# Optimization experiments

Hardware: AMD Instinct MI355X
Metric: run time of the kernel (lower is better)

The kernel has to match this reference:

```python
import jax, jax.numpy as jnp
import numpy as np

NODES, NFEAT = 128, 256


def setup_inputs() -> dict:
    key = jax.random.key(0)
    k1, k2, k3, k4, k5, k6 = jax.random.split(key, 6)
    B = 512
    x = jax.random.normal(k1, (B, NODES, NFEAT), dtype=jnp.float32)
    adj = jax.random.uniform(k2, (B, NODES, NODES), dtype=jnp.float32)
    # GraphConvolution(nfeat, nfeat): weight [nfeat, nfeat], bias [nfeat]
    s = 1.0 / np.sqrt(NFEAT)
    gcn_w = jax.random.uniform(k3, (NFEAT, NFEAT), minval=-s, maxval=s, dtype=jnp.float32)
    gcn_b = jax.random.uniform(k4, (NFEAT,), minval=-s, maxval=s, dtype=jnp.float32)
    # fc: Linear(nfeat*nodes, nfeat), torch layout [out, in]
    s2 = 1.0 / np.sqrt(NFEAT * NODES)
    fc_w = jax.random.uniform(k5, (NFEAT, NFEAT * NODES), minval=-s2, maxval=s2, dtype=jnp.float32)
    fc_b = jax.random.uniform(k6, (NFEAT,), minval=-s2, maxval=s2, dtype=jnp.float32)
    return {"x": x, "adj": adj, "gcn_w": gcn_w, "gcn_b": gcn_b, "fc_w": fc_w, "fc_b": fc_b}


def reference(x, adj, gcn_w, gcn_b, fc_w, fc_b):
    B = x.shape[0]
    # Per-sample loop GCN fused as batched matmuls:
    # support = X @ W ; out = A @ support + b
    support = jnp.einsum('bnf,fg->bng', x, gcn_w)          # [B, nodes, nfeat]
    mid = jnp.einsum('bnm,bmg->bng', adj, support) + gcn_b  # [B, nodes, nfeat]
    # cat along dim0 then reshape(-1, nfeat*nodes) == per-graph flatten
    flat = mid.reshape(B, NODES * NFEAT)
    output = flat @ fc_w.T + fc_b                           # [B, nfeat]
    useful_input = x[:, 0, :]                               # [B, nfeat]
    return (output, useful_input, output)
```

## Files before the change

kernel.cpp:

```cpp
#include <hip/hip_runtime.h>

#define NODES 128
#define NFEAT 256
#define BATCH 512
#define KTOT  (NODES * NFEAT)
#define SPLIT 64
#define KCH   (KTOT / SPLIT)

typedef __bf16 bf16_t;
typedef bf16_t bf16x4 __attribute__((ext_vector_type(4)));
typedef bf16_t bf16x8 __attribute__((ext_vector_type(8)));
typedef float  f32x4  __attribute__((ext_vector_type(4)));

#define BK    32
#define LDK   40
#define BK2   64
#define LDK2  72
#define TILE  128

__device__ __forceinline__ void bar() {
    asm volatile("s_waitcnt lgkmcnt(0)\n\ts_barrier" ::: "memory");
}

__device__ __forceinline__ bf16x8 cvt8(const float4 a, const float4 b) {
    bf16x8 t;
    t[0] = (bf16_t)a.x; t[1] = (bf16_t)a.y; t[2] = (bf16_t)a.z; t[3] = (bf16_t)a.w;
    t[4] = (bf16_t)b.x; t[5] = (bf16_t)b.y; t[6] = (bf16_t)b.z; t[7] = (bf16_t)b.w;
    return t;
}

struct XT { float4 v[4]; };
__device__ __forceinline__ void xload(const float* __restrict__ src, int ld, int k0,
                                      int tid, XT& t) {
#pragma unroll
    for (int i = 0; i < 2; i++) {
        int f = tid + i * 256, r = f >> 2, c = f & 3;
        t.v[2 * i]     = *(const float4*)(src + (size_t)r * ld + k0 + c * 8);
        t.v[2 * i + 1] = *(const float4*)(src + (size_t)r * ld + k0 + c * 8 + 4);
    }
}
__device__ __forceinline__ void xstore(bf16_t* __restrict__ dst, int tid, const XT& t) {
#pragma unroll
    for (int i = 0; i < 2; i++) {
        int f = tid + i * 256, r = f >> 2, c = f & 3;
        *(bf16x8*)(dst + r * LDK + c * 8) = cvt8(t.v[2 * i], t.v[2 * i + 1]);
    }
}

struct XT2 { float4 v[8]; };
__device__ __forceinline__ void xload2(const float* __restrict__ src, int ld, int k0,
                                       int tid, XT2& t) {
#pragma unroll
    for (int i = 0; i < 4; i++) {
        int f = tid + i * 256, r = f >> 3, c = f & 7;
        t.v[2 * i]     = *(const float4*)(src + (size_t)r * ld + k0 + c * 8);
        t.v[2 * i + 1] = *(const float4*)(src + (size_t)r * ld + k0 + c * 8 + 4);
    }
}
__device__ __forceinline__ void xstore2(bf16_t* __restrict__ dst, int tid, const XT2& t) {
#pragma unroll
    for (int i = 0; i < 4; i++) {
        int f = tid + i * 256, r = f >> 3, c = f & 7;
        *(bf16x8*)(dst + r * LDK2 + c * 8) = cvt8(t.v[2 * i], t.v[2 * i + 1]);
    }
}

struct AT2 { bf16x8 v[4]; };
__device__ __forceinline__ void aload2(const bf16_t* __restrict__ src, int ld, int k0,
                                       int tid, AT2& t) {
#pragma unroll
    for (int i = 0; i < 4; i++) {
        int f = tid + i * 256, r = f >> 3, c = f & 7;
        t.v[i] = *(const bf16x8*)(src + (size_t)r * ld + k0 + c * 8);
    }
}
__device__ __forceinline__ void astore2(bf16_t* __restrict__ dst, int tid, const AT2& t) {
#pragma unroll
    for (int i = 0; i < 4; i++) {
        int f = tid + i * 256, r = f >> 3, c = f & 7;
        *(bf16x8*)(dst + r * LDK2 + c * 8) = t.v[i];
    }
}

__global__ __launch_bounds__(256)
void k_wt(const float* __restrict__ w, bf16_t* __restrict__ wT) {
    const int g0 = blockIdx.x * 4;
    const int k  = threadIdx.x;
    const float4 v = *(const float4*)(w + (size_t)k * NFEAT + g0);
    wT[(size_t)(g0 + 0) * NFEAT + k] = (bf16_t)v.x;
    wT[(size_t)(g0 + 1) * NFEAT + k] = (bf16_t)v.y;
    wT[(size_t)(g0 + 2) * NFEAT + k] = (bf16_t)v.z;
    wT[(size_t)(g0 + 3) * NFEAT + k] = (bf16_t)v.w;
}

__global__ __launch_bounds__(256, 3)
void k_fused12(const float* __restrict__ x, const float* __restrict__ adj,
               const bf16_t* __restrict__ wT, const float* __restrict__ gcn_b,
               bf16_t* __restrict__ mid) {
    __shared__ __align__(16) bf16_t As[2][TILE * LDK];
    __shared__ __align__(16) bf16_t Sb[TILE * TILE];
    const int n0  = blockIdx.x * TILE;
    const int b   = blockIdx.y;
    const int tid = threadIdx.x;
    const int lane = tid & 63, w = tid >> 6, wm = w & 1, wn = w >> 1;
    const int l15 = lane & 15, q = lane >> 4;
    const float* xb   = x   + (size_t)b * NODES * NFEAT;
    const float* adjb = adj + (size_t)b * NODES * NODES;

    const bf16_t* wrow[4];
#pragma unroll
    for (int j = 0; j < 4; j++)
        wrow[j] = wT + (size_t)(n0 + wn * 64 + j * 16 + l15) * NFEAT + q * 8;

    f32x4 acc[4][4] = {};
    {
        XT r[3];
        xload(xb, NFEAT, 0 * BK, tid, r[0]);
        xload(xb, NFEAT, 1 * BK, tid, r[1]);
        xload(xb, NFEAT, 2 * BK, tid, r[2]);
        xstore(As[0], tid, r[0]);
        bar();
#pragma unroll
        for (int k = 0; k < 8; k++) {
            if (k + 3 < 8) xload(xb, NFEAT, (k + 3) * BK, tid, r[k % 3]);
            bf16x8 bcur[4];
#pragma unroll
            for (int j = 0; j < 4; j++) bcur[j] = *(const bf16x8*)(wrow[j] + k * BK);
            bf16x8 a[4];
#pragma unroll
            for (int i = 0; i < 4; i++)
                a[i] = *(const bf16x8*)(&As[k & 1][(wm * 64 + i * 16 + l15) * LDK + q * 8]);
#pragma unroll
            for (int i = 0; i < 4; i++)
#pragma unroll
                for (int j = 0; j < 4; j++)
                    acc[i][j] = __builtin_amdgcn_mfma_f32_16x16x32_bf16(a[i], bcur[j], acc[i][j], 0, 0, 0);
            if (k + 1 < 8) xstore(As[(k + 1) & 1], tid, r[(k + 1) % 3]);
            bar();
        }
    }

    XT r[3];
    xload(adjb, NODES, 0 * BK, tid, r[0]);
    xload(adjb, NODES, 1 * BK, tid, r[1]);
    xload(adjb, NODES, 2 * BK, tid, r[2]);
#pragma unroll
    for (int i = 0; i < 4; i++)
#pragma unroll
        for (int j = 0; j < 4; j++)
#pragma unroll
            for (int rr = 0; rr < 4; rr++) {
                int m = wm * 64 + i * 16 + q * 4 + rr;
                int g = wn * 64 + j * 16 + l15;
                int slot = (m >> 3) ^ (g & 15);
                Sb[g * 128 + slot * 8 + (m & 7)] = (bf16_t)acc[i][j][rr];
            }
    bar();
    xstore(As[0], tid, r[0]);
    bar();

    f32x4 acc2[4][4] = {};
#pragma unroll
    for (int k = 0; k < 4; k++) {
        if (k + 3 < 4) xload(adjb, NODES, (k + 3) * BK, tid, r[k % 3]);
        bf16x8 a[4], bb[4];
#pragma unroll
        for (int i = 0; i < 4; i++)
            a[i] = *(const bf16x8*)(&As[k & 1][(wm * 64 + i * 16 + l15) * LDK + q * 8]);
#pragma unroll
        for (int j = 0; j < 4; j++) {
            int R = wn * 64 + j * 16 + l15;
            int slot = (k * 4 + q) ^ (R & 15);
            bb[j] = *(const bf16x8*)(&Sb[R * 128 + slot * 8]);
        }
#pragma unroll
        for (int i = 0; i < 4; i++)
#pragma unroll
            for (int j = 0; j < 4; j++)
                acc2[i][j] = __builtin_amdgcn_mfma_f32_16x16x32_bf16(a[i], bb[j], acc2[i][j], 0, 0, 0);
        if (k + 1 < 4) xstore(As[(k + 1) & 1], tid, r[(k + 1) % 3]);
        bar();
    }
    bf16_t* outb = mid + (size_t)b * NODES * NFEAT;
#pragma unroll
    for (int j = 0; j < 4; j++) {
        int g = n0 + wn * 64 + j * 16 + l15;
        float bias = gcn_b[g];
#pragma unroll
        for (int i = 0; i < 4; i++)
#pragma unroll
            for (int rr = 0; rr < 4; rr++) {
                int node = wm * 64 + i * 16 + q * 4 + rr;
                outb[(size_t)node * NFEAT + g] = (bf16_t)(acc2[i][j][rr] + bias);
            }
    }
}

__global__ __launch_bounds__(256, 2)
void k_out(const bf16_t* __restrict__ flat, const float* __restrict__ fcw,
           bf16_t* __restrict__ part) {
    __shared__ __align__(16) bf16_t As[2][TILE * LDK2];
    __shared__ __align__(16) bf16_t Bs[2][TILE * LDK2];
    const int m0 = blockIdx.x * TILE;
    const int n0 = blockIdx.y * TILE;
    const int kb = blockIdx.z * KCH;
    const int tid = threadIdx.x;
    const int lane = tid & 63, w = tid >> 6, wm = w & 1, wn = w >> 1;
    const int l15 = lane & 15, q = lane >> 4;
    f32x4 acc[4][4] = {};
    const bf16_t* fa = flat + (size_t)m0 * KTOT;
    const float*  fb = fcw + (size_t)n0 * KTOT;

    AT2 ra[3]; XT2 rb[2];
    aload2(fa, KTOT, kb + 0 * BK2, tid, ra[0]);
    xload2(fb, KTOT, kb + 0 * BK2, tid, rb[0]);
    aload2(fa, KTOT, kb + 1 * BK2, tid, ra[1]);
    xload2(fb, KTOT, kb + 1 * BK2, tid, rb[1]);
    aload2(fa, KTOT, kb + 2 * BK2, tid, ra[2]);
    astore2(As[0], tid, ra[0]);
    xstore2(Bs[0], tid, rb[0]);
    bar();
#pragma unroll
    for (int k = 0; k < 8; k++) {
        if (k + 3 < 8) aload2(fa, KTOT, kb + (k + 3) * BK2, tid, ra[k % 3]);
        if (k + 2 < 8) xload2(fb, KTOT, kb + (k + 2) * BK2, tid, rb[k & 1]);
#pragma unroll
        for (int kk = 0; kk < BK2; kk += BK) {
            bf16x8 a[4], bbf[4];
#pragma unroll
            for (int i = 0; i < 4; i++)
                a[i] = *(const bf16x8*)(&As[k & 1][(wm * 64 + i * 16 + l15) * LDK2 + kk + q * 8]);
#pragma unroll
            for (int j = 0; j < 4; j++)
                bbf[j] = *(const bf16x8*)(&Bs[k & 1][(wn * 64 + j * 16 + l15) * LDK2 + kk + q * 8]);
#pragma unroll
            for (int i = 0; i < 4; i++)
#pragma unroll
                for (int j = 0; j < 4; j++)
                    acc[i][j] = __builtin_amdgcn_mfma_f32_16x16x32_bf16(a[i], bbf[j], acc[i][j], 0, 0, 0);
        }
        if (k + 1 < 8) {
            astore2(As[(k + 1) & 1], tid, ra[(k + 1) % 3]);
            xstore2(Bs[(k + 1) & 1], tid, rb[(k + 1) & 1]);
        }
        bar();
    }
    bf16_t* pb = part + (size_t)blockIdx.z * BATCH * NFEAT;
#pragma unroll
    for (int i = 0; i < 4; i++)
#pragma unroll
        for (int j = 0; j < 4; j++)
#pragma unroll
            for (int r = 0; r < 4; r++) {
                int bt_ = m0 + wm * 64 + i * 16 + q * 4 + r;
                int o   = n0 + wn * 64 + j * 16 + l15;
                pb[(size_t)bt_ * NFEAT + o] = (bf16_t)acc[i][j][r];
            }
}

__global__ __launch_bounds__(256)
void k_reduce(const bf16_t* __restrict__ part, const float* __restrict__ fc_b,
              const float* __restrict__ x, float* __restrict__ out) {
    const int g4 = (blockIdx.x * 256 + threadIdx.x) * 4;
    const int o = g4 & (NFEAT - 1), b = g4 >> 8;
    float s[4];
    const float4 c0 = *(const float4*)(fc_b + o);
    s[0] = c0.x; s[1] = c0.y; s[2] = c0.z; s[3] = c0.w;
#pragma unroll 8
    for (int i = 0; i < SPLIT; i++) {
        bf16x4 p = *(const bf16x4*)(part + (size_t)i * BATCH * NFEAT + g4);
#pragma unroll
        for (int j = 0; j < 4; j++) s[j] += (float)p[j];
    }
    float4 o0 = make_float4(s[0], s[1], s[2], s[3]);
    *(float4*)(out + g4) = o0;
    *(float4*)(out + 2 * BATCH * NFEAT + g4) = o0;
    *(float4*)(out + BATCH * NFEAT + g4) = *(const float4*)(x + (size_t)b * NODES * NFEAT + o);
}

extern "C" void kernel_launch(void* const* d_in, const int* in_sizes, int n_in,
                              void* d_out, int out_size, void* d_ws, size_t ws_size,
                              hipStream_t stream) {
    const float* x     = (const float*)d_in[0];
    const float* adj   = (const float*)d_in[1];
    const float* gcn_w = (const float*)d_in[2];
    const float* gcn_b = (const float*)d_in[3];
    const float* fc_w  = (const float*)d_in[4];
    const float* fc_b  = (const float*)d_in[5];
    float* out = (float*)d_out;

    bf16_t* wT   = (bf16_t*)d_ws;
    bf16_t* mid  = (bf16_t*)((char*)d_ws + 131072);
    bf16_t* part = (bf16_t*)((char*)d_ws + 131072 + (size_t)BATCH * NODES * NFEAT * 2);

    k_wt     <<<dim3(64), dim3(256), 0, stream>>>(gcn_w, wT);
    k_fused12<<<dim3(2, BATCH), dim3(256), 0, stream>>>(x, adj, wT, gcn_b, mid);
    k_out    <<<dim3(4, 2, SPLIT), dim3(256), 0, stream>>>(mid, fc_w, part);
    k_reduce <<<dim3(128), dim3(256), 0, stream>>>(part, fc_b, x, out);
}
```

Before: 199.9 us.

## Pre-convert fc weight to bf16, XCD-aware block mapping, register-fed adj operand

The fc weight is converted to bf16 once in a prep kernel, so the split-K output GEMM reads half the bytes and uses a smaller-LDS kernel at higher occupancy with a 128-way split-K. The fused GCN kernel maps blocks so batches are grouped per XCD, loads adj operands straight into registers instead of staging them through LDS, and writes support with vector stores. The reduce kernel splits the partial sums across half-waves and combines them with a shuffle. The changes add an extra fc_w conversion pass each call, a larger workspace, and more partial-sum traffic when the 128-way split path is taken.

```diff
diff --git a/kernel.cpp b/kernel.cpp
--- a/kernel.cpp
+++ b/kernel.cpp
@@ -4,8 +4,6 @@
 #define NFEAT 256
 #define BATCH 512
 #define KTOT  (NODES * NFEAT)
-#define SPLIT 64
-#define KCH   (KTOT / SPLIT)
 
 typedef __bf16 bf16_t;
 typedef bf16_t bf16x4 __attribute__((ext_vector_type(4)));
@@ -14,6 +12,7 @@
 
 #define BK    32
 #define LDK   40
+#define LDK3  36
 #define BK2   64
 #define LDK2  72
 #define TILE  128
@@ -64,7 +63,6 @@
         *(bf16x8*)(dst + r * LDK2 + c * 8) = cvt8(t.v[2 * i], t.v[2 * i + 1]);
     }
 }
-
 struct AT2 { bf16x8 v[4]; };
 __device__ __forceinline__ void aload2(const bf16_t* __restrict__ src, int ld, int k0,
                                        int tid, AT2& t) {
@@ -83,8 +81,20 @@
 }
 
 __global__ __launch_bounds__(256)
-void k_wt(const float* __restrict__ w, bf16_t* __restrict__ wT) {
-    const int g0 = blockIdx.x * 4;
+void k_prep(const float* __restrict__ w, bf16_t* __restrict__ wT,
+            const float* __restrict__ fcw, bf16_t* __restrict__ fcwb, int nconv) {
+    const int bid = blockIdx.x;
+    if (bid < nconv) {
+        const size_t base = ((size_t)bid * 256 + threadIdx.x) * 16;
+        const float4 a0 = *(const float4*)(fcw + base);
+        const float4 a1 = *(const float4*)(fcw + base + 4);
+        const float4 a2 = *(const float4*)(fcw + base + 8);
+        const float4 a3 = *(const float4*)(fcw + base + 12);
+        *(bf16x8*)(fcwb + base)     = cvt8(a0, a1);
+        *(bf16x8*)(fcwb + base + 8) = cvt8(a2, a3);
+        return;
+    }
+    const int g0 = (bid - nconv) * 4;
     const int k  = threadIdx.x;
     const float4 v = *(const float4*)(w + (size_t)k * NFEAT + g0);
     wT[(size_t)(g0 + 0) * NFEAT + k] = (bf16_t)v.x;
@@ -93,14 +103,18 @@
     wT[(size_t)(g0 + 3) * NFEAT + k] = (bf16_t)v.w;
 }
 
-__global__ __launch_bounds__(256, 3)
+__global__ __launch_bounds__(256, 4)
 void k_fused12(const float* __restrict__ x, const float* __restrict__ adj,
                const bf16_t* __restrict__ wT, const float* __restrict__ gcn_b,
                bf16_t* __restrict__ mid) {
-    __shared__ __align__(16) bf16_t As[2][TILE * LDK];
-    __shared__ __align__(16) bf16_t Sb[TILE * TILE];
-    const int n0  = blockIdx.x * TILE;
-    const int b   = blockIdx.y;
+    __shared__ __align__(16) bf16_t smem[TILE * 128];
+    bf16_t* Sb = smem;
+#define AS(bf) (smem + (bf) * (TILE * LDK))
+
+    const int id  = blockIdx.x;
+    const int xcd = id & 7, jj = id >> 3;
+    const int b   = (xcd << 6) | (jj >> 1);
+    const int n0  = (jj & 1) * TILE;
     const int tid = threadIdx.x;
     const int lane = tid & 63, w = tid >> 6, wm = w & 1, wn = w >> 1;
     const int l15 = lane & 15, q = lane >> 4;
@@ -118,7 +132,7 @@
         xload(xb, NFEAT, 0 * BK, tid, r[0]);
         xload(xb, NFEAT, 1 * BK, tid, r[1]);
         xload(xb, NFEAT, 2 * BK, tid, r[2]);
-        xstore(As[0], tid, r[0]);
+        xstore(AS(0), tid, r[0]);
         bar();
 #pragma unroll
         for (int k = 0; k < 8; k++) {
@@ -129,44 +143,55 @@
             bf16x8 a[4];
 #pragma unroll
             for (int i = 0; i < 4; i++)
-                a[i] = *(const bf16x8*)(&As[k & 1][(wm * 64 + i * 16 + l15) * LDK + q * 8]);
+                a[i] = *(const bf16x8*)(AS(k & 1) + (wm * 64 + i * 16 + l15) * LDK + q * 8);
 #pragma unroll
             for (int i = 0; i < 4; i++)
 #pragma unroll
                 for (int j = 0; j < 4; j++)
                     acc[i][j] = __builtin_amdgcn_mfma_f32_16x16x32_bf16(a[i], bcur[j], acc[i][j], 0, 0, 0);
-            if (k + 1 < 8) xstore(As[(k + 1) & 1], tid, r[(k + 1) % 3]);
+            if (k + 1 < 8) xstore(AS((k + 1) & 1), tid, r[(k + 1) % 3]);
             bar();
         }
     }
 
-    XT r[3];
-    xload(adjb, NODES, 0 * BK, tid, r[0]);
-    xload(adjb, NODES, 1 * BK, tid, r[1]);
-    xload(adjb, NODES, 2 * BK, tid, r[2]);
+    const float* aa = adjb + (size_t)(wm * 64 + l15) * NODES + q * 8;
+    float4 p0[4][2];
+#pragma unroll
+    for (int i = 0; i < 4; i++) {
+        p0[i][0] = *(const float4*)(aa + (size_t)i * 16 * NODES);
+        p0[i][1] = *(const float4*)(aa + (size_t)i * 16 * NODES + 4);
+    }
+
 #pragma unroll
     for (int i = 0; i < 4; i++)
 #pragma unroll
-        for (int j = 0; j < 4; j++)
-#pragma unroll
-            for (int rr = 0; rr < 4; rr++) {
-                int m = wm * 64 + i * 16 + q * 4 + rr;
-                int g = wn * 64 + j * 16 + l15;
-                int slot = (m >> 3) ^ (g & 15);
-                Sb[g * 128 + slot * 8 + (m & 7)] = (bf16_t)acc[i][j][rr];
+        for (int j = 0; j < 4; j++) {
+            int m = wm * 64 + i * 16 + q * 4;
+            int g = wn * 64 + j * 16 + l15;
+            int slot = (m >> 3) ^ (g & 15);
+            bf16x4 v;
+            v[0] = (bf16_t)acc[i][j][0]; v[1] = (bf16_t)acc[i][j][1];
+            v[2] = (bf16_t)acc[i][j][2]; v[3] = (bf16_t)acc[i][j][3];
+            *(bf16x4*)(&Sb[g * 128 + slot * 8 + (m & 7)]) = v;
+        }
+    bf16x8 pb[2][4];
+#pragma unroll
+    for (int i = 0; i < 4; i++) pb[0][i] = cvt8(p0[i][0], p0[i][1]);
+    bar();
+
+    f32x4 acc2[4][4] = {};
+#pragma unroll
+    for (int k = 0; k < 4; k++) {
+        const int cur = k & 1, nxt = cur ^ 1;
+        if (k < 3) {
+#pragma unroll
+            for (int i = 0; i < 4; i++) {
+                float4 u = *(const float4*)(aa + (size_t)i * 16 * NODES + (k + 1) * 32);
+                float4 v = *(const float4*)(aa + (size_t)i * 16 * NODES + (k + 1) * 32 + 4);
+                pb[nxt][i] = cvt8(u, v);
             }
-    bar();
-    xstore(As[0], tid, r[0]);
-    bar();
-
-    f32x4 acc2[4][4] = {};
-#pragma unroll
-    for (int k = 0; k < 4; k++) {
-        if (k + 3 < 4) xload(adjb, NODES, (k + 3) * BK, tid, r[k % 3]);
-        bf16x8 a[4], bb[4];
-#pragma unroll
-        for (int i = 0; i < 4; i++)
-            a[i] = *(const bf16x8*)(&As[k & 1][(wm * 64 + i * 16 + l15) * LDK + q * 8]);
+        }
+        bf16x8 bb[4];
 #pragma unroll
         for (int j = 0; j < 4; j++) {
             int R = wn * 64 + j * 16 + l15;
@@ -177,10 +202,9 @@
         for (int i = 0; i < 4; i++)
 #pragma unroll
             for (int j = 0; j < 4; j++)
-                acc2[i][j] = __builtin_amdgcn_mfma_f32_16x16x32_bf16(a[i], bb[j], acc2[i][j], 0, 0, 0);
-        if (k + 1 < 4) xstore(As[(k + 1) & 1], tid, r[(k + 1) % 3]);
-        bar();
-    }
+                acc2[i][j] = __builtin_amdgcn_mfma_f32_16x16x32_bf16(pb[cur][i], bb[j], acc2[i][j], 0, 0, 0);
+    }
+
     bf16_t* outb = mid + (size_t)b * NODES * NFEAT;
 #pragma unroll
     for (int j = 0; j < 4; j++) {
@@ -194,16 +218,84 @@
                 outb[(size_t)node * NFEAT + g] = (bf16_t)(acc2[i][j][rr] + bias);
             }
     }
+#undef AS
+}
+
+template<int NITER>
+__global__ __launch_bounds__(256, 4)
+void k_out_bf(const bf16_t* __restrict__ flat, const bf16_t* __restrict__ fcwb,
+              bf16_t* __restrict__ part) {
+    __shared__ __align__(16) bf16_t As[2][TILE * LDK3];
+    __shared__ __align__(16) bf16_t Bs[2][TILE * LDK3];
+    const int d = blockIdx.x;
+    const int c = d & 7, s = d >> 3;
+    const int xy = s & 7, zhi = s >> 3;
+    const int z  = zhi * 8 + c;
+    const int m0 = (xy & 3) * TILE, n0 = (xy >> 2) * TILE;
+    const int kb = z * (NITER * 32);
+    const int tid = threadIdx.x;
+    const int lane = tid & 63, w = tid >> 6, wm = w & 1, wn = w >> 1;
+    const int l15 = lane & 15, q = lane >> 4;
+    const int sr = tid >> 1, sc = tid & 1;
+    const bf16_t* fa = flat + (size_t)(m0 + sr) * KTOT + kb + sc * 16;
+    const bf16_t* fb = fcwb + (size_t)(n0 + sr) * KTOT + kb + sc * 16;
+    const int sadr = sr * LDK3 + sc * 16;
+
+    struct L { bf16x8 lo, hi; };
+    L ra[2], rb[2];
+#define GLD(dst, p, t) { (dst).lo = *(const bf16x8*)((p) + (t) * 32); \
+                         (dst).hi = *(const bf16x8*)((p) + (t) * 32 + 8); }
+#define SST(base, v)   { *(bf16x8*)(base) = (v).lo; *(bf16x8*)((base) + 8) = (v).hi; }
+
+    f32x4 acc[4][4] = {};
+    GLD(ra[0], fa, 0); GLD(rb[0], fb, 0);
+    GLD(ra[1], fa, 1); GLD(rb[1], fb, 1);
+    SST(&As[0][sadr], ra[0]); SST(&Bs[0][sadr], rb[0]);
+    bar();
+#pragma unroll
+    for (int t = 0; t < NITER; t++) {
+        if (t + 2 < NITER) { GLD(ra[t & 1], fa, t + 2); GLD(rb[t & 1], fb, t + 2); }
+        bf16x8 a[4], bq[4];
+#pragma unroll
+        for (int i = 0; i < 4; i++)
+            a[i] = *(const bf16x8*)(&As[t & 1][(wm * 64 + i * 16 + l15) * LDK3 + q * 8]);
+#pragma unroll
+        for (int j = 0; j < 4; j++)
+            bq[j] = *(const bf16x8*)(&Bs[t & 1][(wn * 64 + j * 16 + l15) * LDK3 + q * 8]);
+#pragma unroll
+        for (int i = 0; i < 4; i++)
+#pragma unroll
+            for (int j = 0; j < 4; j++)
+                acc[i][j] = __builtin_amdgcn_mfma_f32_16x16x32_bf16(a[i], bq[j], acc[i][j], 0, 0, 0);
+        if (t + 1 < NITER) {
+            SST(&As[(t + 1) & 1][sadr], ra[(t + 1) & 1]);
+            SST(&Bs[(t + 1) & 1][sadr], rb[(t + 1) & 1]);
+        }
+        bar();
+    }
+#undef GLD
+#undef SST
+    bf16_t* pb = part + (size_t)z * BATCH * NFEAT;
+#pragma unroll
+    for (int i = 0; i < 4; i++)
+#pragma unroll
+        for (int j = 0; j < 4; j++)
+#pragma unroll
+            for (int r = 0; r < 4; r++) {
+                int bt_ = m0 + wm * 64 + i * 16 + q * 4 + r;
+                int o   = n0 + wn * 64 + j * 16 + l15;
+                pb[(size_t)bt_ * NFEAT + o] = (bf16_t)acc[i][j][r];
+            }
 }
 
 __global__ __launch_bounds__(256, 2)
-void k_out(const bf16_t* __restrict__ flat, const float* __restrict__ fcw,
-           bf16_t* __restrict__ part) {
+void k_out_f32(const bf16_t* __restrict__ flat, const float* __restrict__ fcw,
+               bf16_t* __restrict__ part) {
     __shared__ __align__(16) bf16_t As[2][TILE * LDK2];
     __shared__ __align__(16) bf16_t Bs[2][TILE * LDK2];
     const int m0 = blockIdx.x * TILE;
     const int n0 = blockIdx.y * TILE;
-    const int kb = blockIdx.z * KCH;
+    const int kb = blockIdx.z * (KTOT / 64);
     const int tid = threadIdx.x;
     const int lane = tid & 63, w = tid >> 6, wm = w & 1, wn = w >> 1;
     const int l15 = lane & 15, q = lane >> 4;
@@ -225,7 +317,7 @@
         if (k + 3 < 8) aload2(fa, KTOT, kb + (k + 3) * BK2, tid, ra[k % 3]);
         if (k + 2 < 8) xload2(fb, KTOT, kb + (k + 2) * BK2, tid, rb[k & 1]);
 #pragma unroll
-        for (int kk = 0; kk < BK2; kk += BK) {
+        for (int kk = 0; kk < BK2; kk += 32) {
             bf16x8 a[4], bbf[4];
 #pragma unroll
             for (int i = 0; i < 4; i++)
@@ -258,24 +350,32 @@
             }
 }
 
+template<int NSPL>
 __global__ __launch_bounds__(256)
 void k_reduce(const bf16_t* __restrict__ part, const float* __restrict__ fc_b,
               const float* __restrict__ x, float* __restrict__ out) {
-    const int g4 = (blockIdx.x * 256 + threadIdx.x) * 4;
-    const int o = g4 & (NFEAT - 1), b = g4 >> 8;
-    float s[4];
-    const float4 c0 = *(const float4*)(fc_b + o);
-    s[0] = c0.x; s[1] = c0.y; s[2] = c0.z; s[3] = c0.w;
+    const int gt = blockIdx.x * 256 + threadIdx.x;
+    const int wv = gt >> 6, l = gt & 63, h = l >> 5, li = l & 31;
+    const int p = wv * 32 + li;
+    const int g4 = p * 4, o = g4 & (NFEAT - 1), b = g4 >> 8;
+    float s0 = 0, s1 = 0, s2 = 0, s3 = 0;
+    const bf16_t* pp = part + (size_t)(h * (NSPL / 2)) * BATCH * NFEAT + g4;
 #pragma unroll 8
-    for (int i = 0; i < SPLIT; i++) {
-        bf16x4 p = *(const bf16x4*)(part + (size_t)i * BATCH * NFEAT + g4);
-#pragma unroll
-        for (int j = 0; j < 4; j++) s[j] += (float)p[j];
-    }
-    float4 o0 = make_float4(s[0], s[1], s[2], s[3]);
-    *(float4*)(out + g4) = o0;
-    *(float4*)(out + 2 * BATCH * NFEAT + g4) = o0;
-    *(float4*)(out + BATCH * NFEAT + g4) = *(const float4*)(x + (size_t)b * NODES * NFEAT + o);
+    for (int i = 0; i < NSPL / 2; i++) {
+        bf16x4 v = *(const bf16x4*)(pp + (size_t)i * BATCH * NFEAT);
+        s0 += (float)v[0]; s1 += (float)v[1]; s2 += (float)v[2]; s3 += (float)v[3];
+    }
+    s0 += __shfl_xor(s0, 32); s1 += __shfl_xor(s1, 32);
+    s2 += __shfl_xor(s2, 32); s3 += __shfl_xor(s3, 32);
+    if (h == 0) {
+        const float4 cb = *(const float4*)(fc_b + o);
+        float4 r = make_float4(s0 + cb.x, s1 + cb.y, s2 + cb.z, s3 + cb.w);
+        *(float4*)(out + g4) = r;
+        *(float4*)(out + 2 * BATCH * NFEAT + g4) = r;
+    } else {
+        *(float4*)(out + BATCH * NFEAT + g4) =
+            *(const float4*)(x + (size_t)b * NODES * NFEAT + o);
+    }
 }
 
 extern "C" void kernel_launch(void* const* d_in, const int* in_sizes, int n_in,
@@ -289,12 +389,33 @@
     const float* fc_b  = (const float*)d_in[5];
     float* out = (float*)d_out;
 
+    const size_t midB   = (size_t)BATCH * NODES * NFEAT * 2;
+    const size_t fcwB   = (size_t)NFEAT * KTOT * 2;
+    const size_t p128B  = (size_t)128 * BATCH * NFEAT * 2;
+    const size_t p64B   = p128B / 2;
+
+    int spl;
+    if      (ws_size >= 131072 + midB + p128B + fcwB) spl = 128;
+    else if (ws_size >= 131072 + midB + p64B  + fcwB) spl = 64;
+    else                                              spl = 0;
+
     bf16_t* wT   = (bf16_t*)d_ws;
     bf16_t* mid  = (bf16_t*)((char*)d_ws + 131072);
-    bf16_t* part = (bf16_t*)((char*)d_ws + 131072 + (size_t)BATCH * NODES * NFEAT * 2);
-
-    k_wt     <<<dim3(64), dim3(256), 0, stream>>>(gcn_w, wT);
-    k_fused12<<<dim3(2, BATCH), dim3(256), 0, stream>>>(x, adj, wT, gcn_b, mid);
-    k_out    <<<dim3(4, 2, SPLIT), dim3(256), 0, stream>>>(mid, fc_w, part);
-    k_reduce <<<dim3(128), dim3(256), 0, stream>>>(part, fc_b, x, out);
-}
+    bf16_t* part = (bf16_t*)((char*)d_ws + 131072 + midB);
+    const size_t partB = (spl == 128) ? p128B : p64B;
+    bf16_t* fcwb = (bf16_t*)((char*)d_ws + 131072 + midB + partB);
+
+    const int nconv = spl ? 2048 : 0;
+    k_prep   <<<dim3(nconv + 64), dim3(256), 0, stream>>>(gcn_w, wT, fc_w, fcwb, nconv);
+    k_fused12<<<dim3(1024), dim3(256), 0, stream>>>(x, adj, wT, gcn_b, mid);
+    if (spl == 128) {
+        k_out_bf<8> <<<dim3(1024), dim3(256), 0, stream>>>(mid, fcwb, part);
+        k_reduce<128><<<dim3(256), dim3(256), 0, stream>>>(part, fc_b, x, out);
+    } else if (spl == 64) {
+        k_out_bf<16><<<dim3(512), dim3(256), 0, stream>>>(mid, fcwb, part);
+        k_reduce<64> <<<dim3(256), dim3(256), 0, stream>>>(part, fc_b, x, out);
+    } else {
+        k_out_f32<<<dim3(4, 2, 64), dim3(256), 0, stream>>>(mid, fc_w, part);
+        k_reduce<64> <<<dim3(256), dim3(256), 0, stream>>>(part, fc_b, x, out);
+    }
+}
```

New measurement: 257.7 us. +28.9%, slower.
